# Kernel tuning notes

Hardware: AMD Instinct MI355X
Metric: run time of the kernel (lower is better)

The kernel has to match this reference:

```python
import jax, jax.numpy as jnp
import numpy as np

N_NODES = 100000
N_EDGES = 1600000
IN_DIM = 128
HID = 64
OUT_DIM = 3


def _glorot(key, shape):
    fan_in, fan_out = shape[0], shape[1]
    std = (2.0 / (fan_in + fan_out)) ** 0.5
    return jax.random.normal(key, shape, jnp.float32) * std


def setup_inputs() -> dict:
    key = jax.random.key(0)
    ks = jax.random.split(key, 12)
    x = jax.random.normal(ks[0], (N_NODES, IN_DIM), jnp.float32)
    edge_index = jax.random.randint(ks[1], (2, N_EDGES), 0, N_NODES, dtype=jnp.int32)
    return {
        "x": x,
        "edge_index": edge_index,
        "W1": _glorot(ks[2], (IN_DIM, HID)), "b1": jnp.zeros((HID,), jnp.float32),
        "W2": _glorot(ks[3], (HID, HID)), "b2": jnp.zeros((HID,), jnp.float32),
        "W3": _glorot(ks[4], (HID, HID)), "b3": jnp.zeros((HID,), jnp.float32),
        "W4": _glorot(ks[5], (HID, HID // 2)), "b4": jnp.zeros((HID // 2,), jnp.float32),
        "Wh": _glorot(ks[6], (HID // 2, OUT_DIM)), "bh": jnp.zeros((OUT_DIM,), jnp.float32),
    }


def reference(x, edge_index, W1, b1, W2, b2, W3, b3, W4, b4, Wh, bh):
    n = x.shape[0]
    self_loops = jnp.arange(n, dtype=edge_index.dtype)
    src = jnp.concatenate([edge_index[0], self_loops])  # message sources j
    dst = jnp.concatenate([edge_index[1], self_loops])  # aggregation targets i
    # symmetric GCN normalization with self-loops: deg over targets (unit edge weights)
    deg = jax.ops.segment_sum(jnp.ones_like(dst, jnp.float32), dst, num_segments=n)
    dinv = jnp.where(deg > 0, jax.lax.rsqrt(deg), 0.0)
    norm = dinv[src] * dinv[dst]  # [E+N]

    def gcn(h, W, b):
        h = h @ W  # transform first (PyG GCNConv order)
        agg = jax.ops.segment_sum(h[src] * norm[:, None], dst, num_segments=n)
        return agg + b

    h = jax.nn.relu(gcn(x, W1, b1))   # dropout is identity in eval mode
    h = jax.nn.relu(gcn(h, W2, b2))
    h = jax.nn.relu(gcn(h, W3, b3))
    h = jax.nn.relu(gcn(h, W4, b4))
    return h @ Wh + bh  # [N, 3]
```

## Files before the change

### kernel.cpp

```cpp
#include <hip/hip_runtime.h>
#include <hip/hip_bf16.h>
#include <hip/hip_fp16.h>
#include <cstdint>


#define MAXD 512
#define EB   8192
#define CH   4
#define PADSLACK 4096

__device__ __forceinline__ void hist_body(const int* __restrict__ ei,
                                          int* __restrict__ histM, int E, int b) {
    __shared__ int hist[MAXD];
    const int tid = threadIdx.x;
    hist[tid] = 0; hist[tid + 256] = 0;
    __syncthreads();
    const int base = b * EB;
#pragma unroll 2
    for (int it = 0; it < EB / 256; it += 4) {
        int d[4]; bool ok[4];
#pragma unroll
        for (int u = 0; u < 4; ++u) {
            int e = base + (it + u) * 256 + tid;
            ok[u] = e < E;
            d[u] = ok[u] ? ei[E + e] : 0;
        }
#pragma unroll
        for (int u = 0; u < 4; ++u)
            if (ok[u]) atomicAdd(&hist[d[u] >> 8], 1);
    }
    __syncthreads();
    histM[(size_t)b * MAXD + tid] = hist[tid];
    histM[(size_t)b * MAXD + tid + 256] = hist[tid + 256];
}

__global__ __launch_bounds__(256) void scan_digits_k(int* __restrict__ histM,
                                                     int* __restrict__ totals,
                                                     int NBLK) {
    __shared__ int s[256];
    const int t = threadIdx.x, dg = blockIdx.x;
    int v = (t < NBLK) ? histM[(size_t)t * MAXD + dg] : 0;
    s[t] = v;
    __syncthreads();
    for (int off = 1; off < 256; off <<= 1) {
        int x = (t >= off) ? s[t - off] : 0;
        __syncthreads();
        s[t] += x;
        __syncthreads();
    }
    if (t < NBLK) histM[(size_t)t * MAXD + dg] = s[t] - v;
    if (t == 255) totals[dg] = s[255];
}

__global__ __launch_bounds__(512) void scan_base_k(const int* __restrict__ totals,
                                                   int* __restrict__ cb, int ND) {
    __shared__ int s[512];
    const int t = threadIdx.x;
    int v = (t < ND) ? totals[t] : 0;
    s[t] = v;
    __syncthreads();
    for (int off = 1; off < 512; off <<= 1) {
        int x = (t >= off) ? s[t - off] : 0;
        __syncthreads();
        s[t] += x;
        __syncthreads();
    }
    if (t < ND) cb[t] = s[t] - v;
    if (t == 511) cb[ND] = s[511];
}

template <int K, int OUT, bool HALF_OUT>
__device__ __forceinline__ void gemm_body(const float* __restrict__ H,
                                          const float* __restrict__ W,
                                          const float* __restrict__ dinv,
                                          void* __restrict__ Tout, int n, int bx) {
    constexpr int TX  = OUT / 4;
    constexpr int TY  = 256 / TX;
    constexpr int BM  = TY * 4;
    constexpr int BK  = 32;
    constexpr int PAD = 4;

    __shared__ float At[BK][BM + PAD];
    __shared__ float Ws[BK][OUT];

    const int t    = threadIdx.x;
    const int cx   = t % TX;
    const int ry   = t / TX;
    const int row0 = bx * BM;

    float acc[4][4] = {{0.f}};
    const int arow = t >> 3;
    const int af4  = t & 7;

    for (int k0 = 0; k0 < K; k0 += BK) {
#pragma unroll
        for (int p = 0; p < BM / 32; ++p) {
            int r  = arow + p * 32;
            int gr = row0 + r;
            int grc = gr < n ? gr : n - 1;
            float4 v = *reinterpret_cast<const float4*>(
                H + (size_t)grc * K + k0 + af4 * 4);
            At[af4 * 4 + 0][r] = v.x;
            At[af4 * 4 + 1][r] = v.y;
            At[af4 * 4 + 2][r] = v.z;
            At[af4 * 4 + 3][r] = v.w;
        }
#pragma unroll
        for (int p = 0; p < (BK * OUT) / 1024; ++p) {
            int idx = t + p * 256;
            int wk  = idx / (OUT / 4);
            int wf  = idx % (OUT / 4);
            float4 v = *reinterpret_cast<const float4*>(
                W + (size_t)(k0 + wk) * OUT + wf * 4);
            *reinterpret_cast<float4*>(&Ws[wk][wf * 4]) = v;
        }
        __syncthreads();
#pragma unroll
        for (int k = 0; k < BK; ++k) {
            float4 a = *reinterpret_cast<const float4*>(&At[k][ry * 4]);
            float4 w = *reinterpret_cast<const float4*>(&Ws[k][cx * 4]);
            acc[0][0] = fmaf(a.x, w.x, acc[0][0]);
            acc[0][1] = fmaf(a.x, w.y, acc[0][1]);
            acc[0][2] = fmaf(a.x, w.z, acc[0][2]);
            acc[0][3] = fmaf(a.x, w.w, acc[0][3]);
            acc[1][0] = fmaf(a.y, w.x, acc[1][0]);
            acc[1][1] = fmaf(a.y, w.y, acc[1][1]);
            acc[1][2] = fmaf(a.y, w.z, acc[1][2]);
            acc[1][3] = fmaf(a.y, w.w, acc[1][3]);
            acc[2][0] = fmaf(a.z, w.x, acc[2][0]);
            acc[2][1] = fmaf(a.z, w.y, acc[2][1]);
            acc[2][2] = fmaf(a.z, w.z, acc[2][2]);
            acc[2][3] = fmaf(a.z, w.w, acc[2][3]);
            acc[3][0] = fmaf(a.w, w.x, acc[3][0]);
            acc[3][1] = fmaf(a.w, w.y, acc[3][1]);
            acc[3][2] = fmaf(a.w, w.z, acc[3][2]);
            acc[3][3] = fmaf(a.w, w.w, acc[3][3]);
        }
        __syncthreads();
    }
#pragma unroll
    for (int i = 0; i < 4; ++i) {
        int gr = row0 + ry * 4 + i;
        if (gr < n) {
            if constexpr (HALF_OUT) {
                float di = dinv[gr];
                union { ushort4 u; __half h[4]; } pk;
                pk.h[0] = __float2half_rn(acc[i][0] * di);
                pk.h[1] = __float2half_rn(acc[i][1] * di);
                pk.h[2] = __float2half_rn(acc[i][2] * di);
                pk.h[3] = __float2half_rn(acc[i][3] * di);
                *reinterpret_cast<ushort4*>(
                    (__half*)Tout + (size_t)gr * 64 + cx * 4) = pk.u;
            } else {
                float4 v = make_float4(acc[i][0], acc[i][1], acc[i][2], acc[i][3]);
                *reinterpret_cast<float4*>(
                    (float*)Tout + (size_t)gr * OUT + cx * 4) = v;
            }
        }
    }
}

__device__ __forceinline__ void pack_body(const int* __restrict__ ei,
                                          const int* __restrict__ histM,
                                          const int* __restrict__ cb,
                                          int* __restrict__ packed,
                                          int E, int ND, int b) {
    __shared__ int cur[MAXD];
    const int tid = threadIdx.x;
    for (int t = tid; t < ND; t += 256)
        cur[t] = cb[t] + histM[(size_t)(b * CH) * MAXD + t];
    __syncthreads();
    const int base = b * (CH * EB);
    for (int it = 0; it < (CH * EB) / 256; it += 4) {
        int s[4], d[4]; bool ok[4];
#pragma unroll
        for (int u = 0; u < 4; ++u) {
            int e = base + (it + u) * 256 + tid;
            ok[u] = e < E;
            if (ok[u]) { s[u] = ei[e]; d[u] = ei[E + e]; }
        }
#pragma unroll
        for (int u = 0; u < 4; ++u) {
            if (ok[u]) {
                int pos = atomicAdd(&cur[d[u] >> 8], 1);
                packed[pos] = (s[u] << 8) | (d[u] & 255);
            }
        }
    }
}

__global__ __launch_bounds__(256) void hist_gemm1_k(
    const int* __restrict__ ei, int* __restrict__ histM, int E,
    const float* __restrict__ x, const float* __restrict__ W1,
    float* __restrict__ T1, int n, int NH) {
    const int bx = blockIdx.x;
    if (bx < NH) hist_body(ei, histM, E, bx);
    else         gemm_body<128, 64, false>(x, W1, nullptr, T1, n, bx - NH);
}

__global__ __launch_bounds__(256) void pack_gemm1_k(
    const int* __restrict__ ei, const int* __restrict__ histM,
    const int* __restrict__ cb, int* __restrict__ packed,
    const float* __restrict__ x, const float* __restrict__ W1,
    float* __restrict__ T1, int n, int E, int ND, int NPB, int G1) {
    const int bx = blockIdx.x;
    if (bx < NPB) pack_body(ei, histM, cb, packed, E, ND, bx);
    else          gemm_body<128, 64, false>(x, W1, nullptr, T1, n, G1 + bx - NPB);
}

__global__ __launch_bounds__(256) void bucket_k(const int* __restrict__ packed,
                                                const int* __restrict__ cb,
                                                int* __restrict__ col,
                                                int* __restrict__ rowptr,
                                                int* __restrict__ counts,
                                                float* __restrict__ dinv,
                                                const float* __restrict__ Traw,
                                                __half* __restrict__ Th, int n) {
    __shared__ int   hist[256];
    __shared__ int   pref[256];
    __shared__ int   cur[256];
    __shared__ float dinv_l[256];

    const int tid   = threadIdx.x;
    const int dg    = blockIdx.x;
    const int base  = cb[dg];
    const int m     = cb[dg + 1] - base;
    const int basep = base + dg * PADSLACK;

    hist[tid] = 0;
    __syncthreads();
    for (int k0 = 0; k0 < m; k0 += 1024) {
        int v[4]; bool ok[4];
#pragma unroll
        for (int u = 0; u < 4; ++u) {
            int k = k0 + u * 256 + tid;
            ok[u] = k < m;
            v[u] = ok[u] ? packed[base + k] : 0;
        }
#pragma unroll
        for (int u = 0; u < 4; ++u)
            if (ok[u]) atomicAdd(&hist[v[u] & 255], 1);
    }
    __syncthreads();
    const int deg   = hist[tid];
    const int cnt_p = (deg + 16) & ~15;
    pref[tid] = cnt_p;
    __syncthreads();
    for (int off = 1; off < 256; off <<= 1) {
        int x = (tid >= off) ? pref[tid - off] : 0;
        __syncthreads();
        pref[tid] += x;
        __syncthreads();
    }
    const int rp = basep + pref[tid] - cnt_p;
    const float di = rsqrtf((float)(deg + 1));
    dinv_l[tid] = di;
    cur[tid] = rp + 1;
    const int d = dg * 256 + tid;
    if (d < n) {
        counts[d] = cnt_p;
        dinv[d]   = di;
        rowptr[d] = rp;
        col[rp]   = d;
        for (int k = deg + 1; k < cnt_p; ++k) col[rp + k] = n;
    }
    __syncthreads();
    for (int k0 = 0; k0 < m; k0 += 1024) {
        int v[4]; bool ok[4];
#pragma unroll
        for (int u = 0; u < 4; ++u) {
            int k = k0 + u * 256 + tid;
            ok[u] = k < m;
            v[u] = ok[u] ? packed[base + k] : 0;
        }
#pragma unroll
        for (int u = 0; u < 4; ++u) {
            if (ok[u]) {
                int pos = atomicAdd(&cur[v[u] & 255], 1);
                col[pos] = v[u] >> 8;
            }
        }
    }
    const int r0 = dg * 256;
#pragma unroll 4
    for (int it = 0; it < 16; ++it) {
        int idx = it * 256 + tid;
        int rl  = idx >> 4;
        int r   = r0 + rl;
        if (r < n) {
            float4 v = reinterpret_cast<const float4*>(Traw)[(size_t)r * 16 + (idx & 15)];
            float dd = dinv_l[rl];
            union { ushort4 u; __half h[4]; } pk;
            pk.h[0] = __float2half_rn(v.x * dd);
            pk.h[1] = __float2half_rn(v.y * dd);
            pk.h[2] = __float2half_rn(v.z * dd);
            pk.h[3] = __float2half_rn(v.w * dd);
            reinterpret_cast<ushort4*>(Th)[(size_t)r * 16 + (idx & 15)] = pk.u;
        }
    }
    if (dg == 0 && tid < 16) {
        uint2 z; z.x = 0u; z.y = 0u;
        reinterpret_cast<uint2*>(Th)[(size_t)n * 16 + tid] = z;
    }
}

template <int K, int OUT>
__global__ __launch_bounds__(256) void gemm_h_k(const float* __restrict__ H,
                                                const float* __restrict__ W,
                                                const float* __restrict__ dinv,
                                                __half* __restrict__ T, int n) {
    gemm_body<K, OUT, true>(H, W, dinv, T, n, blockIdx.x);
}

template <int LR, bool FUSE_HEAD>
__global__ __launch_bounds__(256) void agg_k(const __half* __restrict__ T,
                                             const int* __restrict__ rowptr,
                                             const int* __restrict__ counts,
                                             const int* __restrict__ col,
                                             const float* __restrict__ dinv,
                                             const float* __restrict__ bias,
                                             float* __restrict__ O, int n,
                                             const float* __restrict__ Wh,
                                             const float* __restrict__ bh) {
    constexpr int NSW = 64 / LR;
    constexpr int U   = 16 / NSW;
    const int lane = threadIdx.x & 63;
    const int q    = lane % LR;
    const int sw   = lane / LR;
    const int i = (blockIdx.x * blockDim.x + threadIdx.x) >> 6;
    if (i >= n) return;

    const int start = rowptr[i];
    const int cnt   = counts[i];
    const uint2* __restrict__ T2 = reinterpret_cast<const uint2*>(T);

    float4 acc = make_float4(0.f, 0.f, 0.f, 0.f);
    for (int base = 0; base < cnt; base += 64) {
        const int m = min(64, cnt - base);
        int c_l = col[start + base + lane];
        for (int jg = 0; jg < m; jg += 16) {
            int cc[U]; uint2 v[U];
#pragma unroll
            for (int u = 0; u < U; ++u)
                cc[u] = __shfl(c_l, jg + u * NSW + sw, 64);
#pragma unroll
            for (int u = 0; u < U; ++u) v[u] = T2[(size_t)cc[u] * 16 + q];
#pragma unroll
            for (int u = 0; u < U; ++u) {
                const __half2* h2 = reinterpret_cast<const __half2*>(&v[u]);
                float2 f0 = __half22float2(h2[0]);
                float2 f1 = __half22float2(h2[1]);
                acc.x += f0.x; acc.y += f0.y; acc.z += f1.x; acc.w += f1.y;
            }
        }
    }
#pragma unroll
    for (int off = LR; off < 64; off <<= 1) {
        acc.x += __shfl_xor(acc.x, off, 64);
        acc.y += __shfl_xor(acc.y, off, 64);
        acc.z += __shfl_xor(acc.z, off, 64);
        acc.w += __shfl_xor(acc.w, off, 64);
    }
    const float di = dinv[i];
    const float4 b4 = reinterpret_cast<const float4*>(bias)[q];
    float4 h;
    h.x = fmaxf(fmaf(di, acc.x, b4.x), 0.f);
    h.y = fmaxf(fmaf(di, acc.y, b4.y), 0.f);
    h.z = fmaxf(fmaf(di, acc.z, b4.z), 0.f);
    h.w = fmaxf(fmaf(di, acc.w, b4.w), 0.f);
    if constexpr (!FUSE_HEAD) {
        if (sw == 0)
            reinterpret_cast<float4*>(O + (size_t)i * 64)[q] = h;
    } else {
        float p0 = h.x * Wh[(4 * q + 0) * 3 + 0];
        float p1 = h.x * Wh[(4 * q + 0) * 3 + 1];
        float p2 = h.x * Wh[(4 * q + 0) * 3 + 2];
        p0 = fmaf(h.y, Wh[(4 * q + 1) * 3 + 0], p0);
        p1 = fmaf(h.y, Wh[(4 * q + 1) * 3 + 1], p1);
        p2 = fmaf(h.y, Wh[(4 * q + 1) * 3 + 2], p2);
        p0 = fmaf(h.z, Wh[(4 * q + 2) * 3 + 0], p0);
        p1 = fmaf(h.z, Wh[(4 * q + 2) * 3 + 1], p1);
        p2 = fmaf(h.z, Wh[(4 * q + 2) * 3 + 2], p2);
        p0 = fmaf(h.w, Wh[(4 * q + 3) * 3 + 0], p0);
        p1 = fmaf(h.w, Wh[(4 * q + 3) * 3 + 1], p1);
        p2 = fmaf(h.w, Wh[(4 * q + 3) * 3 + 2], p2);
#pragma unroll
        for (int off = 1; off < LR; off <<= 1) {
            p0 += __shfl_xor(p0, off, 64);
            p1 += __shfl_xor(p1, off, 64);
            p2 += __shfl_xor(p2, off, 64);
        }
        if (lane == 0) {
            O[(size_t)i * 3 + 0] = p0 + bh[0];
            O[(size_t)i * 3 + 1] = p1 + bh[1];
            O[(size_t)i * 3 + 2] = p2 + bh[2];
        }
    }
}

extern "C" void kernel_launch(void* const* d_in, const int* in_sizes, int n_in,
                              void* d_out, int out_size, void* d_ws, size_t ws_size,
                              hipStream_t stream) {
    const float* x  = (const float*)d_in[0];
    const int*   ei = (const int*)d_in[1];
    const float* W1 = (const float*)d_in[2];
    const float* b1 = (const float*)d_in[3];
    const float* W2 = (const float*)d_in[4];
    const float* b2 = (const float*)d_in[5];
    const float* W3 = (const float*)d_in[6];
    const float* b3 = (const float*)d_in[7];
    const float* W4 = (const float*)d_in[8];
    const float* b4 = (const float*)d_in[9];
    const float* Wh = (const float*)d_in[10];
    const float* bh = (const float*)d_in[11];
    float* out = (float*)d_out;

    const int n = in_sizes[0] / 128;
    const int E = in_sizes[1] / 2;
    const int ND   = (n + 255) / 256;
    const int NBLK = (E + EB - 1) / EB;
    const int NPB  = (NBLK + CH - 1) / CH;

    char* ws = (char*)d_ws;
    auto alloc = [&](size_t bytes) {
        char* p = ws;
        ws += (bytes + 255) & ~(size_t)255;
        return p;
    };
    int*    histM  = (int*)alloc((size_t)NBLK * MAXD * 4);
    int*    totals = (int*)alloc((size_t)MAXD * 4);
    int*    cbA    = (int*)alloc((size_t)(MAXD + 1) * 4);
    int*    packed = (int*)alloc((size_t)E * 4);
    int*    col    = (int*)alloc(((size_t)E + (size_t)ND * PADSLACK + 256) * 4);
    int*    rowptr = (int*)alloc((size_t)n * 4);
    int*    counts = (int*)alloc((size_t)n * 4);
    float*  dinv   = (float*)alloc((size_t)n * 4);
    float*  bufF   = (float*)alloc((size_t)n * 64 * 4);
    __half* bufH   = (__half*)alloc(((size_t)n + 1) * 64 * 2);

    dim3 blk(256);
    const int G  = (n + 63) / 64;
    const int G1 = G / 3;
    const int G2 = G - G1;
    const int agg_blocks = (n + 3) / 4;

    hist_gemm1_k<<<dim3(NBLK + G1), blk, 0, stream>>>(ei, histM, E, x, W1, bufF, n, NBLK);
    scan_digits_k<<<dim3(ND), blk, 0, stream>>>(histM, totals, NBLK);
    scan_base_k<<<dim3(1), dim3(512), 0, stream>>>(totals, cbA, ND);
    pack_gemm1_k<<<dim3(NPB + G2), blk, 0, stream>>>(ei, histM, cbA, packed,
                                                     x, W1, bufF, n, E, ND, NPB, G1);
    bucket_k<<<dim3(ND), blk, 0, stream>>>(packed, cbA, col, rowptr, counts,
                                           dinv, bufF, bufH, n);
    agg_k<16, false><<<dim3(agg_blocks), blk, 0, stream>>>(
        bufH, rowptr, counts, col, dinv, b1, bufF, n, nullptr, nullptr);
    gemm_h_k<64, 64><<<dim3(G), blk, 0, stream>>>(bufF, W2, dinv, bufH, n);
    agg_k<16, false><<<dim3(agg_blocks), blk, 0, stream>>>(
        bufH, rowptr, counts, col, dinv, b2, bufF, n, nullptr, nullptr);
    gemm_h_k<64, 64><<<dim3(G), blk, 0, stream>>>(bufF, W3, dinv, bufH, n);
    agg_k<16, false><<<dim3(agg_blocks), blk, 0, stream>>>(
        bufH, rowptr, counts, col, dinv, b3, bufF, n, nullptr, nullptr);
    gemm_h_k<64, 32><<<dim3((n + 127) / 128), blk, 0, stream>>>(bufF, W4, dinv, bufH, n);
    agg_k<8, true><<<dim3(agg_blocks), blk, 0, stream>>>(
        bufH, rowptr, counts, col, dinv, b4, out, n, Wh, bh);
}
```

Before: 400.3 us.

## Shrink per-row padding to 8 and split pack work into finer blocks

Per-row CSR padding drops from multiples of 16 to multiples of 8. The aggregation loop gains a half-width tail step that handles a final group of 8 neighbours, so fewer padded dummy rows are gathered in each of the four aggregation passes. The pack phase now runs one block per histogram block instead of one per group of four, which raises parallelism at the cost of more small blocks. The per-digit slack reserve is halved to match the smaller padding.

```diff
diff --git a/kernel.cpp b/kernel.cpp
--- a/kernel.cpp
+++ b/kernel.cpp
@@ -6,8 +6,7 @@
 
 #define MAXD 512
 #define EB   8192
-#define CH   4
-#define PADSLACK 4096
+#define PADSLACK 2048
 
 __device__ __forceinline__ void hist_body(const int* __restrict__ ei,
                                           int* __restrict__ histM, int E, int b) {
@@ -168,10 +167,10 @@
     __shared__ int cur[MAXD];
     const int tid = threadIdx.x;
     for (int t = tid; t < ND; t += 256)
-        cur[t] = cb[t] + histM[(size_t)(b * CH) * MAXD + t];
-    __syncthreads();
-    const int base = b * (CH * EB);
-    for (int it = 0; it < (CH * EB) / 256; it += 4) {
+        cur[t] = cb[t] + histM[(size_t)b * MAXD + t];
+    __syncthreads();
+    const int base = b * EB;
+    for (int it = 0; it < EB / 256; it += 4) {
         int s[4], d[4]; bool ok[4];
 #pragma unroll
         for (int u = 0; u < 4; ++u) {
@@ -243,7 +242,7 @@
     }
     __syncthreads();
     const int deg   = hist[tid];
-    const int cnt_p = (deg + 16) & ~15;
+    const int cnt_p = (deg + 8) & ~7;
     pref[tid] = cnt_p;
     __syncthreads();
     for (int off = 1; off < 256; off <<= 1) {
@@ -324,6 +323,7 @@
                                              const float* __restrict__ bh) {
     constexpr int NSW = 64 / LR;
     constexpr int U   = 16 / NSW;
+    constexpr int UH  = U / 2;
     const int lane = threadIdx.x & 63;
     const int q    = lane % LR;
     const int sw   = lane / LR;
@@ -338,7 +338,8 @@
     for (int base = 0; base < cnt; base += 64) {
         const int m = min(64, cnt - base);
         int c_l = col[start + base + lane];
-        for (int jg = 0; jg < m; jg += 16) {
+        int jg = 0;
+        for (; jg + 16 <= m; jg += 16) {
             int cc[U]; uint2 v[U];
 #pragma unroll
             for (int u = 0; u < U; ++u)
@@ -347,6 +348,21 @@
             for (int u = 0; u < U; ++u) v[u] = T2[(size_t)cc[u] * 16 + q];
 #pragma unroll
             for (int u = 0; u < U; ++u) {
+                const __half2* h2 = reinterpret_cast<const __half2*>(&v[u]);
+                float2 f0 = __half22float2(h2[0]);
+                float2 f1 = __half22float2(h2[1]);
+                acc.x += f0.x; acc.y += f0.y; acc.z += f1.x; acc.w += f1.y;
+            }
+        }
+        if (jg < m) {
+            int cc[UH]; uint2 v[UH];
+#pragma unroll
+            for (int u = 0; u < UH; ++u)
+                cc[u] = __shfl(c_l, jg + u * NSW + sw, 64);
+#pragma unroll
+            for (int u = 0; u < UH; ++u) v[u] = T2[(size_t)cc[u] * 16 + q];
+#pragma unroll
+            for (int u = 0; u < UH; ++u) {
                 const __half2* h2 = reinterpret_cast<const __half2*>(&v[u]);
                 float2 f0 = __half22float2(h2[0]);
                 float2 f1 = __half22float2(h2[1]);
@@ -419,7 +435,6 @@
     const int E = in_sizes[1] / 2;
     const int ND   = (n + 255) / 256;
     const int NBLK = (E + EB - 1) / EB;
-    const int NPB  = (NBLK + CH - 1) / CH;
 
     char* ws = (char*)d_ws;
     auto alloc = [&](size_t bytes) {
@@ -447,8 +462,8 @@
     hist_gemm1_k<<<dim3(NBLK + G1), blk, 0, stream>>>(ei, histM, E, x, W1, bufF, n, NBLK);
     scan_digits_k<<<dim3(ND), blk, 0, stream>>>(histM, totals, NBLK);
     scan_base_k<<<dim3(1), dim3(512), 0, stream>>>(totals, cbA, ND);
-    pack_gemm1_k<<<dim3(NPB + G2), blk, 0, stream>>>(ei, histM, cbA, packed,
-                                                     x, W1, bufF, n, E, ND, NPB, G1);
+    pack_gemm1_k<<<dim3(NBLK + G2), blk, 0, stream>>>(ei, histM, cbA, packed,
+                                                      x, W1, bufF, n, E, ND, NBLK, G1);
     bucket_k<<<dim3(ND), blk, 0, stream>>>(packed, cbA, col, rowptr, counts,
                                            dinv, bufF, bufH, n);
     agg_k<16, false><<<dim3(agg_blocks), blk, 0, stream>>>(
```

Measured after the change: 383.9 us. -4.1%, faster.
